# Kernel optimization log

Measured on AMD Instinct MI355X. Metric: run time of the kernel, lower is better.

## Reference

```python
import jax, jax.numpy as jnp
import numpy as np

B, N_PER, DEG, F_IN, F_HID = 64, 1024, 16, 128, 128
E = B * N_PER * DEG  # 1,048,576 edges, grouped per graph


def setup_inputs() -> dict:
    key = jax.random.key(0)
    ks = jax.random.split(key, 16)
    n_total = B * N_PER
    x = jax.random.normal(ks[0], (n_total, F_IN), dtype=jnp.float32)
    # edges are random within each graph block
    local = jax.random.randint(ks[1], (2, E), 0, N_PER)
    offs = (jnp.arange(E, dtype=jnp.int64) // (N_PER * DEG)) * N_PER
    edge_index = (local.astype(jnp.int64) + offs[None, :])
    edge_weight = jax.random.uniform(ks[2], (E,), dtype=jnp.float32)
    batch_index = jnp.repeat(jnp.arange(B, dtype=jnp.int64), N_PER)
    s = 1.0 / np.sqrt(F_HID)
    params = {
        'W1': jax.random.normal(ks[3], (F_IN, F_HID)) * s,
        'b1': jnp.zeros((F_HID,), jnp.float32),
        'p1': jax.random.normal(ks[4], (F_HID,)) * s,
        'W2': jax.random.normal(ks[5], (F_HID, F_HID)) * s,
        'b2': jnp.zeros((F_HID,), jnp.float32),
        'p2': jax.random.normal(ks[6], (F_HID,)) * s,
        'W3': jax.random.normal(ks[7], (F_HID, F_HID)) * s,
        'b3': jnp.zeros((F_HID,), jnp.float32),
        'p3': jax.random.normal(ks[8], (F_HID,)) * s,
        'Wo': jax.random.normal(ks[9], (2 * F_HID, 1)) * s,
        'bo': jnp.zeros((1,), jnp.float32),
    }
    return {'x': x, 'edge_index': edge_index, 'edge_weight': edge_weight,
            'batch_index': batch_index, **params}


def _gcn_conv(x, src, dst, w, W, b):
    # GCNConv with add_self_loops=True, symmetric normalization, edge_weight.
    n = x.shape[0]
    xW = x @ W
    deg = jnp.zeros((n,), x.dtype).at[dst].add(w) + 1.0  # +1 from self-loop fill
    dinv = jax.lax.rsqrt(deg)
    norm = dinv[src] * w * dinv[dst]
    agg = jnp.zeros_like(xW).at[dst].add(norm[:, None] * xW[src])
    return agg + (dinv * dinv)[:, None] * xW + b  # self-loop term + bias


def _topk_pool(x, src, dst, w, p, n, k):
    # TopKPooling with nonlinearity=sigmoid, equal-size graphs (n -> k nodes).
    f = x.shape[1]
    xr = x.reshape(B, n, f)
    score = jax.nn.sigmoid((xr @ p) / jnp.linalg.norm(p))  # [B, n]
    vals, perm = jax.lax.top_k(score, k)                    # per-graph top-k
    xn = jnp.take_along_axis(xr, perm[:, :, None], axis=1) * vals[:, :, None]
    # inverse map old local idx -> new local idx (-1 if dropped)
    inv = jnp.full((B, n), -1, dtype=jnp.int32)
    inv = inv.at[jnp.arange(B)[:, None], perm].set(jnp.arange(k, dtype=jnp.int32)[None, :])
    g = src // n
    sl = inv[g, src % n]
    dl = inv[dst // n, dst % n]
    keep = (sl >= 0) & (dl >= 0)
    # dropped edges are masked to node 0 with weight 0 (contribute nothing)
    src2 = jnp.where(keep, g * k + sl, 0)
    dst2 = jnp.where(keep, (dst // n) * k + dl, 0)
    w2 = jnp.where(keep, w, jnp.zeros((), w.dtype))
    return xn.reshape(B * k, f), src2, dst2, w2


def reference(x, edge_index, edge_weight, batch_index,
              W1, b1, p1, W2, b2, p2, W3, b3, p3, Wo, bo):
    src, dst = edge_index[0], edge_index[1]
    w = edge_weight
    n = N_PER
    h = _gcn_conv(x, src, dst, w, W1, b1)
    h, src, dst, w = _topk_pool(h, src, dst, w, p1, n, n // 2); n //= 2
    h = jax.nn.relu(h)
    h = _gcn_conv(h, src, dst, w, W2, b2)
    h, src, dst, w = _topk_pool(h, src, dst, w, p2, n, n // 2); n //= 2
    h = jax.nn.relu(h)
    h = _gcn_conv(h, src, dst, w, W3, b3)
    h, src, dst, w = _topk_pool(h, src, dst, w, p3, n, n // 2); n //= 2
    h = jax.nn.relu(h)
    hr = h.reshape(B, n, -1)
    cat = jnp.concatenate([hr.max(axis=1), hr.mean(axis=1)], axis=1)  # gmp || gap
    out = jax.nn.sigmoid(cat @ Wo + bo)
    return out, cat
```

## Files before the change

kernel.cpp:

```cpp
#include <hip/hip_runtime.h>

#define NB 64
#define EDGES 1048576
#define NTOT  65536

struct __align__(8) CsrE { int s; float w; };

using bf16x8 = __attribute__((ext_vector_type(8))) short;
using f32x4  = __attribute__((ext_vector_type(4))) float;

__global__ void k_zerof(float* __restrict__ p, int n){
  int i=blockIdx.x*256+threadIdx.x; if(i<n) p[i]=0.f;
}

__device__ inline void split1(float x, unsigned &hi16, unsigned &lo16){
  unsigned b=__float_as_uint(x);
  unsigned h=(b+0x7FFFu+((b>>16)&1u))&0xFFFF0000u;
  float lf=x-__uint_as_float(h);
  unsigned lb=__float_as_uint(lf);
  hi16=h>>16;
  lo16=(lb+0x7FFFu+((lb>>16)&1u))>>16;
}

__device__ inline void split8(const float4&u, const float4&v, bf16x8&hi, bf16x8&lo){
  float e[8]={u.x,u.y,u.z,u.w,v.x,v.y,v.z,v.w};
  #pragma unroll
  for(int j=0;j<8;++j){
    unsigned h16,l16; split1(e[j],h16,l16);
    hi[j]=(short)h16; lo[j]=(short)l16;
  }
}

__global__ __launch_bounds__(256) void k_cntpack(const int* __restrict__ edst,
        const float* __restrict__ ew, int* __restrict__ chunkcnt, float* __restrict__ chunkw,
        const float* __restrict__ W1, const float* __restrict__ W2,
        const float* __restrict__ W3, unsigned* __restrict__ outp){
  __shared__ int lc[1024];
  __shared__ float lw[1024];
  int b=blockIdx.x, tid=threadIdx.x;
  if(b<512){
    int xcd=b&7, slot=b>>3;
    int graph=xcd*8+(slot&7), chunk=slot>>3;
    int e0=graph*16384+chunk*2048;
    for(int t=tid;t<1024;t+=256){ lc[t]=0; lw[t]=0.f; }
    __syncthreads();
    for(int e=e0+tid; e<e0+2048; e+=256){
      int dl=edst[e]&1023;
      atomicAdd(&lc[dl],1);
      atomicAdd(&lw[dl],ew[e]);
    }
    __syncthreads();
    for(int t=tid;t<1024;t+=256){
      chunkcnt[chunk*65536+graph*1024+t]=lc[t];
      chunkw  [chunk*65536+graph*1024+t]=lw[t];
    }
  } else {
    int wb=b-512, m=wb>>3;
    const float* W = (m==0)?W1:((m==1)?W2:W3);
    unsigned* o = outp + m*16384;
    for(int t=(wb&7)*256+tid; t<8192; t+=2048){
      int i=t&3, l=(t>>2)&63, c=(t>>8)&7, q=(t>>11)&3;
      int col=c*16+(l&15);
      int k0=q*32+((l>>4)<<3)+i*2;
      float x0=W[k0*128+col], x1=W[(k0+1)*128+col];
      unsigned h0,l0,h1,l1;
      split1(x0,h0,l0); split1(x1,h1,l1);
      int base=((q*8+c)*2)*256;
      o[base + l*4 + i]       = (h1<<16)|h0;
      o[base + 256 + l*4 + i] = (l1<<16)|l0;
    }
  }
}

__global__ __launch_bounds__(256) void k_mm1scat(const float* __restrict__ X,
        const unsigned* __restrict__ Wpk,
        const int* __restrict__ esrc, const int* __restrict__ edst,
        const float* __restrict__ ew, const int* __restrict__ chunkcnt,
        const float* __restrict__ chunkw, int* __restrict__ rowptr,
        float* __restrict__ dinv1, CsrE* __restrict__ csr,
        float* __restrict__ Y){
  __shared__ __align__(16) unsigned Wl[16384];
  int b=blockIdx.x;
  if(b<512){
    const int RPB=128;
    int row0b=b*RPB;
    for(int t=threadIdx.x;t<4096;t+=256)
      ((uint4*)Wl)[t]=((const uint4*)Wpk)[t];
    const int wave=threadIdx.x>>6, lane=threadIdx.x&63;
    const int row0=row0b+wave*32;
    const int lrow=lane&15, lko=(lane>>4)<<3;
    int orow[2];
    #pragma unroll
    for(int s=0;s<2;++s) orow[s]=row0+s*16+lrow;
    const f32x4 vzero={0.f,0.f,0.f,0.f};
    f32x4 acc[2][8];
    #pragma unroll
    for(int s=0;s<2;++s){
      #pragma unroll
      for(int c=0;c<8;++c) acc[s][c]=vzero;
    }
    __syncthreads();
    const char* wb=(const char*)Wl + lane*16;
    float4 u[2],v[2];
    #pragma unroll
    for(int s=0;s<2;++s){
      const float* xp=X+(size_t)orow[s]*128+lko;
      u[s]=*(const float4*)xp; v[s]=*(const float4*)(xp+4);
    }
    #pragma unroll
    for(int q=0;q<4;++q){
      float4 un[2],vn[2];
      if(q<3){
        #pragma unroll
        for(int s=0;s<2;++s){
          const float* xp=X+(size_t)orow[s]*128+(q+1)*32+lko;
          un[s]=*(const float4*)xp; vn[s]=*(const float4*)(xp+4);
        }
      }
      bf16x8 Ah[2],Al[2];
      #pragma unroll
      for(int s=0;s<2;++s) split8(u[s],v[s],Ah[s],Al[s]);
      #pragma unroll
      for(int c=0;c<8;++c){
        const bf16x8 bh=*(const bf16x8*)(wb + (q*8+c)*2048);
        const bf16x8 bl=*(const bf16x8*)(wb + (q*8+c)*2048 + 1024);
        #pragma unroll
        for(int s=0;s<2;++s){
          acc[s][c]=__builtin_amdgcn_mfma_f32_16x16x32_bf16(Ah[s],bh,acc[s][c],0,0,0);
          acc[s][c]=__builtin_amdgcn_mfma_f32_16x16x32_bf16(Al[s],bh,acc[s][c],0,0,0);
          acc[s][c]=__builtin_amdgcn_mfma_f32_16x16x32_bf16(Ah[s],bl,acc[s][c],0,0,0);
        }
      }
      if(q<3){
        #pragma unroll
        for(int s=0;s<2;++s){ u[s]=un[s]; v[s]=vn[s]; }
      }
    }
    const int dcol=lane&15, dr0=(lane>>4)<<2;
    #pragma unroll
    for(int s=0;s<2;++s){
      #pragma unroll
      for(int c=0;c<8;++c){
        #pragma unroll
        for(int r=0;r<4;++r){
          Y[(size_t)(row0+s*16+dr0+r)*128 + c*16 + dcol]=acc[s][c][r];
        }
      }
    }
  } else {
    int* lc=(int*)Wl;
    int* wsum=(int*)Wl+1024;
    int sb=b-512, i=threadIdx.x;
    int lane=i&63, w=i>>6;
    int xcd=sb&7, slot=sb>>3;
    int graph=xcd*8+(slot&7), chunk=slot>>3;
    int n0=4*i, o0=graph*1024+n0;
    int ck[4][8], csum[4];
    int tot=0;
    #pragma unroll
    for(int j=0;j<4;++j){
      int c=0;
      #pragma unroll
      for(int k=0;k<8;++k){ int t=chunkcnt[k*65536+o0+j]; ck[j][k]=t; c+=t; }
      csum[j]=c; tot+=c;
    }
    int v=tot;
    #pragma unroll
    for(int off=1;off<64;off<<=1){ int t=__shfl_up(v,off,64); if(lane>=off) v+=t; }
    if(lane==63) wsum[w]=v;
    __syncthreads();
    int base=0;
    for(int k=0;k<w;++k) base+=wsum[k];
    int texcl=base+v-tot;
    int run=texcl;
    #pragma unroll
    for(int j=0;j<4;++j){
      int r0=graph*16384+run;
      if(chunk==0){
        rowptr[o0+j]=r0;
        float wsv=0.f;
        #pragma unroll
        for(int k=0;k<8;++k) wsv+=chunkw[k*65536+o0+j];
        dinv1[o0+j]=rsqrtf(wsv+1.0f);
      }
      int myfill=r0;
      #pragma unroll
      for(int k=0;k<8;++k) if(k<chunk) myfill+=ck[j][k];
      lc[n0+j]=myfill;
      run+=csum[j];
    }
    if(graph==63 && chunk==0 && i==255) rowptr[65536]=EDGES;
    __syncthreads();
    int e0=graph*16384+chunk*2048;
    for(int e=e0+i; e<e0+2048; e+=256){
      int dl=edst[e]&1023;
      int pos=atomicAdd(&lc[dl],1);
      CsrE ce; ce.s=esrc[e]; ce.w=ew[e];
      csr[pos]=ce;
    }
  }
}

template<bool G, int S>
__global__ __launch_bounds__(256) void mm_mfma(const float* __restrict__ X,
        const unsigned* __restrict__ Wpk, const int* __restrict__ selold,
        const float* __restrict__ score, float* __restrict__ Y, int gshift){
  __shared__ __align__(16) unsigned Wl[16384];
  const int RPB = 64*S;
  int b=blockIdx.x;
  int row0b;
  if(G){
    int xcd=b&7, slot=b>>3, bpg=1<<gshift;
    int graph=xcd*8+(slot>>gshift), idx=slot&(bpg-1);
    row0b = graph*(bpg*RPB) + idx*RPB;
  } else row0b = b*RPB;
  for(int t=threadIdx.x;t<4096;t+=256)
    ((uint4*)Wl)[t]=((const uint4*)Wpk)[t];
  const int wave=threadIdx.x>>6, lane=threadIdx.x&63;
  const int row0 = row0b + wave*(16*S);
  const int lrow=lane&15, lko=(lane>>4)<<3;
  int orow[S]; float scr[S];
  #pragma unroll
  for(int s=0;s<S;++s){
    int rr=row0+s*16+lrow;
    orow[s]=G?selold[rr]:rr;
    scr[s]=G?score[orow[s]]:1.f;
  }
  const f32x4 vzero={0.f,0.f,0.f,0.f};
  f32x4 acc[S][8];
  #pragma unroll
  for(int s=0;s<S;++s){
    #pragma unroll
    for(int c=0;c<8;++c) acc[s][c]=vzero;
  }
  __syncthreads();
  const char* wb=(const char*)Wl + lane*16;
  float4 u[S],v[S];
  #pragma unroll
  for(int s=0;s<S;++s){
    const float* xp=X+(size_t)orow[s]*128+lko;
    u[s]=*(const float4*)xp; v[s]=*(const float4*)(xp+4);
  }
  #pragma unroll
  for(int q=0;q<4;++q){
    float4 un[S],vn[S];
    if(q<3){
      #pragma unroll
      for(int s=0;s<S;++s){
        const float* xp=X+(size_t)orow[s]*128+(q+1)*32+lko;
        un[s]=*(const float4*)xp; vn[s]=*(const float4*)(xp+4);
      }
    }
    bf16x8 Ah[S],Al[S];
    #pragma unroll
    for(int s=0;s<S;++s){
      if(G){
        u[s].x=fmaxf(u[s].x*scr[s],0.f); u[s].y=fmaxf(u[s].y*scr[s],0.f);
        u[s].z=fmaxf(u[s].z*scr[s],0.f); u[s].w=fmaxf(u[s].w*scr[s],0.f);
        v[s].x=fmaxf(v[s].x*scr[s],0.f); v[s].y=fmaxf(v[s].y*scr[s],0.f);
        v[s].z=fmaxf(v[s].z*scr[s],0.f); v[s].w=fmaxf(v[s].w*scr[s],0.f);
      }
      split8(u[s],v[s],Ah[s],Al[s]);
    }
    #pragma unroll
    for(int c=0;c<8;++c){
      const bf16x8 bh=*(const bf16x8*)(wb + (q*8+c)*2048);
      const bf16x8 bl=*(const bf16x8*)(wb + (q*8+c)*2048 + 1024);
      #pragma unroll
      for(int s=0;s<S;++s){
        acc[s][c]=__builtin_amdgcn_mfma_f32_16x16x32_bf16(Ah[s],bh,acc[s][c],0,0,0);
        acc[s][c]=__builtin_amdgcn_mfma_f32_16x16x32_bf16(Al[s],bh,acc[s][c],0,0,0);
        acc[s][c]=__builtin_amdgcn_mfma_f32_16x16x32_bf16(Ah[s],bl,acc[s][c],0,0,0);
      }
    }
    if(q<3){
      #pragma unroll
      for(int s=0;s<S;++s){ u[s]=un[s]; v[s]=vn[s]; }
    }
  }
  const int dcol=lane&15, dr0=(lane>>4)<<2;
  #pragma unroll
  for(int s=0;s<S;++s){
    #pragma unroll
    for(int c=0;c<8;++c){
      #pragma unroll
      for(int r=0;r<4;++r){
        Y[(size_t)(row0+s*16+dr0+r)*128 + c*16 + dcol]=acc[s][c][r];
      }
    }
  }
}

template<bool F>
__global__ __launch_bounds__(256) void k_gather(const float* __restrict__ xw, const CsrE* __restrict__ csr,
        const int* __restrict__ rowptr, const int* __restrict__ map, const int* __restrict__ inv,
        const float* __restrict__ dinvv, const float* __restrict__ bias, const float* __restrict__ p,
        float* __restrict__ h, float* __restrict__ score, int gshift, int ns){
  int wv=threadIdx.x>>6, half=(threadIdx.x>>5)&1, hl=threadIdx.x&31;
  int b=blockIdx.x, xcd=b&7, slot=b>>3, bpg=1<<gshift;
  int graph=xcd*8+(slot>>gshift), idx=slot&(bpg-1);
  int v = graph*(bpg<<3) + (idx<<3) + wv*2 + half;
  if(v>=ns) return;
  int d0 = F? map[v] : v;
  float dv=dinvv[v];
  int rs=rowptr[d0], re=rowptr[d0+1];
  const int f4=hl*4;
  float4 accA={0.f,0.f,0.f,0.f}, accB={0.f,0.f,0.f,0.f};
  for(int base=rs; base<re; base+=32){
    int len=re-base; if(len>32) len=32;
    int sidx=0; float cf=0.f;
    if(hl<len){
      CsrE en=csr[base+hl];
      int s=en.s; bool live=true;
      if(F){ int t=inv[s]; live=(t>=0); s=live?t:0; }
      if(live){ sidx=s; cf=dinvv[s]*en.w; }
    }
    int len8=(len+7)&~7;
    for(int j=0;j<len8;j+=8){
      float cc[8]; int ss[8];
      #pragma unroll
      for(int m=0;m<8;++m){ cc[m]=__shfl(cf,j+m,32); ss[m]=__shfl(sidx,j+m,32); }
      float4 xv_[8];
      #pragma unroll
      for(int m=0;m<8;++m) xv_[m]=*(const float4*)&xw[(size_t)ss[m]*128+f4];
      #pragma unroll
      for(int m=0;m<8;m+=2){
        accA.x+=cc[m]*xv_[m].x; accA.y+=cc[m]*xv_[m].y;
        accA.z+=cc[m]*xv_[m].z; accA.w+=cc[m]*xv_[m].w;
        accB.x+=cc[m+1]*xv_[m+1].x; accB.y+=cc[m+1]*xv_[m+1].y;
        accB.z+=cc[m+1]*xv_[m+1].z; accB.w+=cc[m+1]*xv_[m+1].w;
      }
    }
  }
  float4 acc; acc.x=accA.x+accB.x; acc.y=accA.y+accB.y;
  acc.z=accA.z+accB.z; acc.w=accA.w+accB.w;
  const float4 xv=*(const float4*)&xw[(size_t)v*128+f4];
  const float4 bv=*(const float4*)&bias[f4];
  float d2=dv*dv;
  float4 hv;
  hv.x=acc.x*dv + d2*xv.x + bv.x;
  hv.y=acc.y*dv + d2*xv.y + bv.y;
  hv.z=acc.z*dv + d2*xv.z + bv.z;
  hv.w=acc.w*dv + d2*xv.w + bv.w;
  *(float4*)&h[(size_t)v*128+f4]=hv;
  const float4 pv=*(const float4*)&p[f4];
  float z=hv.x*pv.x+hv.y*pv.y+hv.z*pv.z+hv.w*pv.w;
  float pp=pv.x*pv.x+pv.y*pv.y+pv.z*pv.z+pv.w*pv.w;
  #pragma unroll
  for(int m=16;m>0;m>>=1){ z+=__shfl_xor(z,m,32); pp+=__shfl_xor(pp,m,32); }
  if(hl==0) score[v]=1.0f/(1.0f+expf(-z/sqrtf(pp)));
}

template<int N, int K, int MODE>
__global__ __launch_bounds__(N) void k_topk(const float* __restrict__ score,
        int* __restrict__ inv, int* __restrict__ selold,
        const int* __restrict__ inv1s, const int* __restrict__ sel1s,
        int* __restrict__ inv12, int* __restrict__ map12,
        const int* __restrict__ rowptr, const CsrE* __restrict__ csr,
        float* __restrict__ dinv_out,
        const float* __restrict__ h3, const float* __restrict__ Wo,
        const float* __restrict__ bo, float* __restrict__ outp){
  __shared__ unsigned hist[256];
  __shared__ int wsum[16];
  __shared__ int c_sh, r_sh;
  __shared__ float red2[256];
  __shared__ int sOld[128];
  __shared__ float sSc[128];
  int g=blockIdx.x, i=threadIdx.x;
  int lane=i&63, w=i>>6;
  int gv=g*N+i;
  unsigned key=__float_as_uint(score[gv]);
  int st=1;
  int R=K;
  #pragma unroll
  for(int pass=0; pass<4; ++pass){
    int shift=24-pass*8;
    if(i<256) hist[i]=0;
    __syncthreads();
    unsigned byte=(key>>shift)&255u;
    if(st==1) atomicAdd(&hist[byte],1u);
    __syncthreads();
    unsigned hcnt=0, sfx=0;
    if(i<256){
      hcnt=hist[i]; sfx=hcnt;
      #pragma unroll
      for(int off=1;off<64;off<<=1){
        unsigned t=__shfl_down(sfx,off,64);
        if(lane+off<64) sfx+=t;
      }
      if(lane==0) wsum[w]=(int)sfx;
    }
    __syncthreads();
    if(i<256){
      int tot=0;
      for(int k=w+1;k<4;++k) tot+=wsum[k];
      int Si=(int)sfx+tot;
      int A=Si-(int)hcnt;
      if(A<R && R<=Si){ c_sh=i; r_sh=R-A; }
    }
    __syncthreads();
    int c=c_sh; R=r_sh;
    if(st==1){
      if((int)byte>c) st=2;
      else if((int)byte<c) st=0;
    }
    __syncthreads();
  }
  int alive=(st==1)?1:0;
  unsigned long long mA=__ballot(alive);
  int rA=__popcll(mA & ((1ULL<<lane)-1ULL));
  if(lane==0) wsum[w]=__popcll(mA);
  __syncthreads();
  int offA=0;
  for(int k=0;k<w;++k) offA+=wsum[k];
  int tie_rank=offA+rA;
  int sel=(st==2)||(st==1 && tie_rank<R);
  __syncthreads();
  unsigned long long mS=__ballot(sel);
  int rS=__popcll(mS & ((1ULL<<lane)-1ULL));
  if(lane==0) wsum[w]=__popcll(mS);
  __syncthreads();
  int offS=0;
  for(int k=0;k<w;++k) offS+=wsum[k];
  int ng=g*K+offS+rS;
  if(sel && ng<NB*K){ inv[gv]=ng; selold[ng]=gv; }
  else inv[gv]=-1;
  if(MODE==1){
    __syncthreads();
    for(int t=i; t<K; t+=N){
      int v=g*K+t;
      int d0=selold[v];
      int rs=rowptr[d0], re=rowptr[d0+1];
      float s0=0.f,s1=0.f,s2=0.f,s3=0.f;
      int e=rs;
      for(; e+4<=re; e+=4){
        CsrE e0=csr[e], e1=csr[e+1], e2=csr[e+2], e3=csr[e+3];
        if(inv[e0.s]>=0) s0+=e0.w;
        if(inv[e1.s]>=0) s1+=e1.w;
        if(inv[e2.s]>=0) s2+=e2.w;
        if(inv[e3.s]>=0) s3+=e3.w;
      }
      for(; e<re; ++e){
        CsrE en=csr[e];
        if(inv[en.s]>=0) s0+=en.w;
      }
      dinv_out[v]=rsqrtf((s0+s1)+(s2+s3)+1.0f);
    }
  }
  if(MODE==2){
    __syncthreads();
    for(int t=i; t<1024; t+=N){
      int v0=g*1024+t;
      int q=inv1s[v0];
      inv12[v0]=(q>=0)?inv[q]:-1;
    }
    for(int t=i; t<K; t+=N){
      int v=g*K+t;
      map12[v]=sel1s[selold[v]];
    }
    __syncthreads();
    for(int t=i; t<K; t+=N){
      int v=g*K+t;
      int d0=map12[v];
      int rs=rowptr[d0], re=rowptr[d0+1];
      float s0=0.f,s1=0.f,s2=0.f,s3=0.f;
      int e=rs;
      for(; e+4<=re; e+=4){
        CsrE e0=csr[e], e1=csr[e+1], e2=csr[e+2], e3=csr[e+3];
        if(inv12[e0.s]>=0) s0+=e0.w;
        if(inv12[e1.s]>=0) s1+=e1.w;
        if(inv12[e2.s]>=0) s2+=e2.w;
        if(inv12[e3.s]>=0) s3+=e3.w;
      }
      for(; e<re; ++e){
        CsrE en=csr[e];
        if(inv12[en.s]>=0) s0+=en.w;
      }
      dinv_out[v]=rsqrtf((s0+s1)+(s2+s3)+1.0f);
    }
  }
  if(MODE==3){
    __syncthreads();
    if(i<128){ int o=selold[g*128+i]; sOld[i]=o; sSc[i]=score[o]; }
    __syncthreads();
    int f=i&127, hf=i>>7;
    float mx=-3.4e38f, sm=0.f;
    #pragma unroll 4
    for(int nd=hf*64; nd<hf*64+64; ++nd){
      float vv=fmaxf(h3[(size_t)sOld[nd]*128+f]*sSc[nd],0.f);
      mx=fmaxf(mx,vv); sm+=vv;
    }
    red2[i]=mx; __syncthreads();
    float mx2 = (hf==0)? fmaxf(mx,red2[i+128]) : 0.f;
    __syncthreads();
    red2[i]=sm; __syncthreads();
    if(hf==0){
      float smT=sm+red2[i+128];
      float mean=smT*(1.0f/128.0f);
      outp[64+g*256+f]    =mx2;
      outp[64+g*256+128+f]=mean;
    }
    __syncthreads();
    if(hf==0) red2[f]=mx2*Wo[f]+( (sm+red2[f+128]) * (1.0f/128.0f))*Wo[128+f];
    __syncthreads();
    for(int off=64;off>0;off>>=1){
      if(i<off) red2[i]+=red2[i+off];
      __syncthreads();
    }
    if(i==0){ float z=red2[0]+bo[0]; outp[g]=1.0f/(1.0f+expf(-z)); }
  }
}

extern "C" void kernel_launch(void* const* d_in, const int* in_sizes, int n_in,
                              void* d_out, int out_size, void* d_ws, size_t ws_size,
                              hipStream_t stream) {
  (void)in_sizes; (void)n_in;
  const float* x  = (const float*)d_in[0];
  const int*   ei = (const int*)d_in[1];
  const float* ew = (const float*)d_in[2];
  const float* W1=(const float*)d_in[4];  const float* b1=(const float*)d_in[5];  const float* p1=(const float*)d_in[6];
  const float* W2=(const float*)d_in[7];  const float* b2=(const float*)d_in[8];  const float* p2=(const float*)d_in[9];
  const float* W3=(const float*)d_in[10]; const float* b3=(const float*)d_in[11]; const float* p3=(const float*)d_in[12];
  const float* Wo=(const float*)d_in[13]; const float* bo=(const float*)d_in[14];
  float* out=(float*)d_out;

  char* ws=(char*)d_ws;
  size_t cur=0;
  float* slot0=(float*)(ws+cur); cur+=33554432;
  float* slot1=(float*)(ws+cur); cur+=33554432;
  CsrE*  csr  =(CsrE*)(ws+cur);  cur+=(size_t)EDGES*8;
  int*   chunkcnt=(int*)(ws+cur); cur+=2097152;
  float* chunkw  =(float*)(ws+cur); cur+=2097152;
  int*   rowptr=(int*) (ws+cur); cur+=262400;
  float* dinv1=(float*)(ws+cur); cur+=262144;
  float* dinv2=(float*)(ws+cur); cur+=131072;
  float* dinv3=(float*)(ws+cur); cur+=65536;
  float* sc1  =(float*)(ws+cur); cur+=262144;
  float* sc2  =(float*)(ws+cur); cur+=131072;
  float* sc3  =(float*)(ws+cur); cur+=65536;
  int*   inv1 =(int*)  (ws+cur); cur+=262144;
  int*   inv2 =(int*)  (ws+cur); cur+=131072;
  int*   invS =(int*)  (ws+cur); cur+=65536;
  int*   inv12=(int*)  (ws+cur); cur+=262144;
  int*   sel1 =(int*)  (ws+cur); cur+=131072;
  int*   sel2 =(int*)  (ws+cur); cur+=65536;
  int*   sel3 =(int*)  (ws+cur); cur+=32768;
  int*   map12=(int*)  (ws+cur); cur+=65536;
  unsigned* wpk=(unsigned*)(ws+cur); cur+=196608;

  if (ws_size < cur) {
    k_zerof<<<(out_size+255)/256,256,0,stream>>>(out,out_size);
    return;
  }

  const int* esrc=ei; const int* edst=ei+EDGES;

  k_cntpack<<<536,256,0,stream>>>(edst,ew,chunkcnt,chunkw,W1,W2,W3,wpk);
  k_mm1scat<<<1024,256,0,stream>>>(x,wpk,esrc,edst,ew,chunkcnt,chunkw,
                                   rowptr,dinv1,csr,slot0);
  k_gather<false><<<NTOT/8,256,0,stream>>>(slot0,csr,rowptr,nullptr,nullptr,
                                           dinv1,b1,p1,slot1,sc1,7,NTOT);
  k_topk<1024,512,1><<<NB,1024,0,stream>>>(sc1,inv1,sel1,nullptr,nullptr,nullptr,nullptr,
                                           rowptr,csr,dinv2,nullptr,nullptr,nullptr,nullptr);

  mm_mfma<true,1><<<32768/64,256,0,stream>>>(slot1,wpk+16384,sel1,sc1,slot0,3);
  k_gather<true><<<32768/8,256,0,stream>>>(slot0,csr,rowptr,sel1,inv1,
                                           dinv2,b2,p2,slot1,sc2,6,32768);
  k_topk<512,256,2><<<NB,512,0,stream>>>(sc2,inv2,sel2,inv1,sel1,inv12,map12,
                                         rowptr,csr,dinv3,nullptr,nullptr,nullptr,nullptr);

  mm_mfma<true,1><<<16384/64,256,0,stream>>>(slot1,wpk+32768,sel2,sc2,slot0,2);
  k_gather<true><<<16384/8,256,0,stream>>>(slot0,csr,rowptr,map12,inv12,
                                           dinv3,b3,p3,slot1,sc3,5,16384);
  k_topk<256,128,3><<<NB,256,0,stream>>>(sc3,invS,sel3,nullptr,nullptr,nullptr,nullptr,
                                         nullptr,nullptr,nullptr,slot1,Wo,bo,out);
}
```

Baseline: 271.8 us.

## Move pooled-degree computation from topk blocks into extra blocks of matmul kernel

The per-node degree/dinv computation for the pooled graphs was done inside the 64-block top-k kernels, where each block serially walked many nodes' edge lists. It now runs in extra thread blocks appended to the following MFMA matmul launch, which spreads the work over many more blocks and lets it overlap with the matmul. The gather inner loop is also narrowed from 8 to 4 edges per step, and the final readout is simplified to one thread per feature. The simpler readout gives up the two-way split over nodes that it had before.

```diff
diff --git a/kernel.cpp b/kernel.cpp
--- a/kernel.cpp
+++ b/kernel.cpp
@@ -201,93 +201,147 @@
   }
 }
 
-template<bool G, int S>
+template<bool G, int S, int EPI, int MMB>
 __global__ __launch_bounds__(256) void mm_mfma(const float* __restrict__ X,
         const unsigned* __restrict__ Wpk, const int* __restrict__ selold,
-        const float* __restrict__ score, float* __restrict__ Y, int gshift){
+        const float* __restrict__ score, float* __restrict__ Y, int gshift,
+        const int* __restrict__ inv1, const int* __restrict__ sel1,
+        const int* __restrict__ inv2, const int* __restrict__ sel2,
+        int* __restrict__ inv12, int* __restrict__ map12,
+        const int* __restrict__ rowptr, const CsrE* __restrict__ csr,
+        float* __restrict__ dinv_out){
   __shared__ __align__(16) unsigned Wl[16384];
-  const int RPB = 64*S;
   int b=blockIdx.x;
-  int row0b;
-  if(G){
-    int xcd=b&7, slot=b>>3, bpg=1<<gshift;
-    int graph=xcd*8+(slot>>gshift), idx=slot&(bpg-1);
-    row0b = graph*(bpg*RPB) + idx*RPB;
-  } else row0b = b*RPB;
-  for(int t=threadIdx.x;t<4096;t+=256)
-    ((uint4*)Wl)[t]=((const uint4*)Wpk)[t];
-  const int wave=threadIdx.x>>6, lane=threadIdx.x&63;
-  const int row0 = row0b + wave*(16*S);
-  const int lrow=lane&15, lko=(lane>>4)<<3;
-  int orow[S]; float scr[S];
-  #pragma unroll
-  for(int s=0;s<S;++s){
-    int rr=row0+s*16+lrow;
-    orow[s]=G?selold[rr]:rr;
-    scr[s]=G?score[orow[s]]:1.f;
-  }
-  const f32x4 vzero={0.f,0.f,0.f,0.f};
-  f32x4 acc[S][8];
-  #pragma unroll
-  for(int s=0;s<S;++s){
-    #pragma unroll
-    for(int c=0;c<8;++c) acc[s][c]=vzero;
-  }
-  __syncthreads();
-  const char* wb=(const char*)Wl + lane*16;
-  float4 u[S],v[S];
-  #pragma unroll
-  for(int s=0;s<S;++s){
-    const float* xp=X+(size_t)orow[s]*128+lko;
-    u[s]=*(const float4*)xp; v[s]=*(const float4*)(xp+4);
-  }
-  #pragma unroll
-  for(int q=0;q<4;++q){
-    float4 un[S],vn[S];
-    if(q<3){
+  if(b<MMB){
+    const int RPB = 64*S;
+    int row0b;
+    if(G){
+      int xcd=b&7, slot=b>>3, bpg=1<<gshift;
+      int graph=xcd*8+(slot>>gshift), idx=slot&(bpg-1);
+      row0b = graph*(bpg*RPB) + idx*RPB;
+    } else row0b = b*RPB;
+    for(int t=threadIdx.x;t<4096;t+=256)
+      ((uint4*)Wl)[t]=((const uint4*)Wpk)[t];
+    const int wave=threadIdx.x>>6, lane=threadIdx.x&63;
+    const int row0 = row0b + wave*(16*S);
+    const int lrow=lane&15, lko=(lane>>4)<<3;
+    int orow[S]; float scr[S];
+    #pragma unroll
+    for(int s=0;s<S;++s){
+      int rr=row0+s*16+lrow;
+      orow[s]=G?selold[rr]:rr;
+      scr[s]=G?score[orow[s]]:1.f;
+    }
+    const f32x4 vzero={0.f,0.f,0.f,0.f};
+    f32x4 acc[S][8];
+    #pragma unroll
+    for(int s=0;s<S;++s){
+      #pragma unroll
+      for(int c=0;c<8;++c) acc[s][c]=vzero;
+    }
+    __syncthreads();
+    const char* wb=(const char*)Wl + lane*16;
+    float4 u[S],v[S];
+    #pragma unroll
+    for(int s=0;s<S;++s){
+      const float* xp=X+(size_t)orow[s]*128+lko;
+      u[s]=*(const float4*)xp; v[s]=*(const float4*)(xp+4);
+    }
+    #pragma unroll
+    for(int q=0;q<4;++q){
+      float4 un[S],vn[S];
+      if(q<3){
+        #pragma unroll
+        for(int s=0;s<S;++s){
+          const float* xp=X+(size_t)orow[s]*128+(q+1)*32+lko;
+          un[s]=*(const float4*)xp; vn[s]=*(const float4*)(xp+4);
+        }
+      }
+      bf16x8 Ah[S],Al[S];
       #pragma unroll
       for(int s=0;s<S;++s){
-        const float* xp=X+(size_t)orow[s]*128+(q+1)*32+lko;
-        un[s]=*(const float4*)xp; vn[s]=*(const float4*)(xp+4);
-      }
-    }
-    bf16x8 Ah[S],Al[S];
+        if(G){
+          u[s].x=fmaxf(u[s].x*scr[s],0.f); u[s].y=fmaxf(u[s].y*scr[s],0.f);
+          u[s].z=fmaxf(u[s].z*scr[s],0.f); u[s].w=fmaxf(u[s].w*scr[s],0.f);
+          v[s].x=fmaxf(v[s].x*scr[s],0.f); v[s].y=fmaxf(v[s].y*scr[s],0.f);
+          v[s].z=fmaxf(v[s].z*scr[s],0.f); v[s].w=fmaxf(v[s].w*scr[s],0.f);
+        }
+        split8(u[s],v[s],Ah[s],Al[s]);
+      }
+      #pragma unroll
+      for(int c=0;c<8;++c){
+        const bf16x8 bh=*(const bf16x8*)(wb + (q*8+c)*2048);
+        const bf16x8 bl=*(const bf16x8*)(wb + (q*8+c)*2048 + 1024);
+        #pragma unroll
+        for(int s=0;s<S;++s){
+          acc[s][c]=__builtin_amdgcn_mfma_f32_16x16x32_bf16(Ah[s],bh,acc[s][c],0,0,0);
+          acc[s][c]=__builtin_amdgcn_mfma_f32_16x16x32_bf16(Al[s],bh,acc[s][c],0,0,0);
+          acc[s][c]=__builtin_amdgcn_mfma_f32_16x16x32_bf16(Ah[s],bl,acc[s][c],0,0,0);
+        }
+      }
+      if(q<3){
+        #pragma unroll
+        for(int s=0;s<S;++s){ u[s]=un[s]; v[s]=vn[s]; }
+      }
+    }
+    const int dcol=lane&15, dr0=(lane>>4)<<2;
     #pragma unroll
     for(int s=0;s<S;++s){
-      if(G){
-        u[s].x=fmaxf(u[s].x*scr[s],0.f); u[s].y=fmaxf(u[s].y*scr[s],0.f);
-        u[s].z=fmaxf(u[s].z*scr[s],0.f); u[s].w=fmaxf(u[s].w*scr[s],0.f);
-        v[s].x=fmaxf(v[s].x*scr[s],0.f); v[s].y=fmaxf(v[s].y*scr[s],0.f);
-        v[s].z=fmaxf(v[s].z*scr[s],0.f); v[s].w=fmaxf(v[s].w*scr[s],0.f);
-      }
-      split8(u[s],v[s],Ah[s],Al[s]);
-    }
-    #pragma unroll
-    for(int c=0;c<8;++c){
-      const bf16x8 bh=*(const bf16x8*)(wb + (q*8+c)*2048);
-      const bf16x8 bl=*(const bf16x8*)(wb + (q*8+c)*2048 + 1024);
-      #pragma unroll
-      for(int s=0;s<S;++s){
-        acc[s][c]=__builtin_amdgcn_mfma_f32_16x16x32_bf16(Ah[s],bh,acc[s][c],0,0,0);
-        acc[s][c]=__builtin_amdgcn_mfma_f32_16x16x32_bf16(Al[s],bh,acc[s][c],0,0,0);
-        acc[s][c]=__builtin_amdgcn_mfma_f32_16x16x32_bf16(Ah[s],bl,acc[s][c],0,0,0);
-      }
-    }
-    if(q<3){
-      #pragma unroll
-      for(int s=0;s<S;++s){ u[s]=un[s]; v[s]=vn[s]; }
-    }
-  }
-  const int dcol=lane&15, dr0=(lane>>4)<<2;
-  #pragma unroll
-  for(int s=0;s<S;++s){
-    #pragma unroll
-    for(int c=0;c<8;++c){
-      #pragma unroll
-      for(int r=0;r<4;++r){
-        Y[(size_t)(row0+s*16+dr0+r)*128 + c*16 + dcol]=acc[s][c][r];
-      }
-    }
+      #pragma unroll
+      for(int c=0;c<8;++c){
+        #pragma unroll
+        for(int r=0;r<4;++r){
+          Y[(size_t)(row0+s*16+dr0+r)*128 + c*16 + dcol]=acc[s][c][r];
+        }
+      }
+    }
+    return;
+  }
+  if(EPI==2){
+    int v=(b-MMB)*256+threadIdx.x;
+    int d0=sel1[v];
+    int rs=rowptr[d0], re=rowptr[d0+1];
+    float s0=0.f,s1=0.f,s2=0.f,s3=0.f;
+    int e=rs;
+    for(; e+4<=re; e+=4){
+      CsrE e0=csr[e], e1=csr[e+1], e2=csr[e+2], e3=csr[e+3];
+      if(inv1[e0.s]>=0) s0+=e0.w;
+      if(inv1[e1.s]>=0) s1+=e1.w;
+      if(inv1[e2.s]>=0) s2+=e2.w;
+      if(inv1[e3.s]>=0) s3+=e3.w;
+    }
+    for(; e<re; ++e){
+      CsrE en=csr[e];
+      if(inv1[en.s]>=0) s0+=en.w;
+    }
+    dinv_out[v]=rsqrtf((s0+s1)+(s2+s3)+1.0f);
+  }
+  if(EPI==3){
+    int g=b-MMB, i=threadIdx.x;
+    for(int t=i; t<1024; t+=256){
+      int v0=g*1024+t;
+      int q=inv1[v0];
+      inv12[v0]=(q>=0)?inv2[q]:-1;
+    }
+    int v=g*256+i;
+    map12[v]=sel1[sel2[v]];
+    __syncthreads();
+    int d0=map12[v];
+    int rs=rowptr[d0], re=rowptr[d0+1];
+    float s0=0.f,s1=0.f,s2=0.f,s3=0.f;
+    int e=rs;
+    for(; e+4<=re; e+=4){
+      CsrE e0=csr[e], e1=csr[e+1], e2=csr[e+2], e3=csr[e+3];
+      if(inv12[e0.s]>=0) s0+=e0.w;
+      if(inv12[e1.s]>=0) s1+=e1.w;
+      if(inv12[e2.s]>=0) s2+=e2.w;
+      if(inv12[e3.s]>=0) s3+=e3.w;
+    }
+    for(; e<re; ++e){
+      CsrE en=csr[e];
+      if(inv12[en.s]>=0) s0+=en.w;
+    }
+    dinv_out[v]=rsqrtf((s0+s1)+(s2+s3)+1.0f);
   }
 }
 
@@ -315,21 +369,20 @@
       if(F){ int t=inv[s]; live=(t>=0); s=live?t:0; }
       if(live){ sidx=s; cf=dinvv[s]*en.w; }
     }
-    int len8=(len+7)&~7;
-    for(int j=0;j<len8;j+=8){
-      float cc[8]; int ss[8];
-      #pragma unroll
-      for(int m=0;m<8;++m){ cc[m]=__shfl(cf,j+m,32); ss[m]=__shfl(sidx,j+m,32); }
-      float4 xv_[8];
-      #pragma unroll
-      for(int m=0;m<8;++m) xv_[m]=*(const float4*)&xw[(size_t)ss[m]*128+f4];
-      #pragma unroll
-      for(int m=0;m<8;m+=2){
-        accA.x+=cc[m]*xv_[m].x; accA.y+=cc[m]*xv_[m].y;
-        accA.z+=cc[m]*xv_[m].z; accA.w+=cc[m]*xv_[m].w;
-        accB.x+=cc[m+1]*xv_[m+1].x; accB.y+=cc[m+1]*xv_[m+1].y;
-        accB.z+=cc[m+1]*xv_[m+1].z; accB.w+=cc[m+1]*xv_[m+1].w;
-      }
+    int len4=(len+3)&~3;
+    for(int j=0;j<len4;j+=4){
+      float c0=__shfl(cf,j,32),   c1=__shfl(cf,j+1,32);
+      float c2=__shfl(cf,j+2,32), c3=__shfl(cf,j+3,32);
+      int   s0=__shfl(sidx,j,32),   s1=__shfl(sidx,j+1,32);
+      int   s2=__shfl(sidx,j+2,32), s3=__shfl(sidx,j+3,32);
+      const float4 x0=*(const float4*)&xw[(size_t)s0*128+f4];
+      const float4 x1=*(const float4*)&xw[(size_t)s1*128+f4];
+      const float4 x2=*(const float4*)&xw[(size_t)s2*128+f4];
+      const float4 x3=*(const float4*)&xw[(size_t)s3*128+f4];
+      accA.x+=c0*x0.x; accA.y+=c0*x0.y; accA.z+=c0*x0.z; accA.w+=c0*x0.w;
+      accB.x+=c1*x1.x; accB.y+=c1*x1.y; accB.z+=c1*x1.z; accB.w+=c1*x1.w;
+      accA.x+=c2*x2.x; accA.y+=c2*x2.y; accA.z+=c2*x2.z; accA.w+=c2*x2.w;
+      accB.x+=c3*x3.x; accB.y+=c3*x3.y; accB.z+=c3*x3.z; accB.w+=c3*x3.w;
     }
   }
   float4 acc; acc.x=accA.x+accB.x; acc.y=accA.y+accB.y;
@@ -354,18 +407,12 @@
 template<int N, int K, int MODE>
 __global__ __launch_bounds__(N) void k_topk(const float* __restrict__ score,
         int* __restrict__ inv, int* __restrict__ selold,
-        const int* __restrict__ inv1s, const int* __restrict__ sel1s,
-        int* __restrict__ inv12, int* __restrict__ map12,
-        const int* __restrict__ rowptr, const CsrE* __restrict__ csr,
-        float* __restrict__ dinv_out,
         const float* __restrict__ h3, const float* __restrict__ Wo,
         const float* __restrict__ bo, float* __restrict__ outp){
   __shared__ unsigned hist[256];
   __shared__ int wsum[16];
   __shared__ int c_sh, r_sh;
-  __shared__ float red2[256];
-  __shared__ int sOld[128];
-  __shared__ float sSc[128];
+  __shared__ float red[128];
   int g=blockIdx.x, i=threadIdx.x;
   int lane=i&63, w=i>>6;
   int gv=g*N+i;
@@ -425,89 +472,27 @@
   int ng=g*K+offS+rS;
   if(sel && ng<NB*K){ inv[gv]=ng; selold[ng]=gv; }
   else inv[gv]=-1;
-  if(MODE==1){
-    __syncthreads();
-    for(int t=i; t<K; t+=N){
-      int v=g*K+t;
-      int d0=selold[v];
-      int rs=rowptr[d0], re=rowptr[d0+1];
-      float s0=0.f,s1=0.f,s2=0.f,s3=0.f;
-      int e=rs;
-      for(; e+4<=re; e+=4){
-        CsrE e0=csr[e], e1=csr[e+1], e2=csr[e+2], e3=csr[e+3];
-        if(inv[e0.s]>=0) s0+=e0.w;
-        if(inv[e1.s]>=0) s1+=e1.w;
-        if(inv[e2.s]>=0) s2+=e2.w;
-        if(inv[e3.s]>=0) s3+=e3.w;
-      }
-      for(; e<re; ++e){
-        CsrE en=csr[e];
-        if(inv[en.s]>=0) s0+=en.w;
-      }
-      dinv_out[v]=rsqrtf((s0+s1)+(s2+s3)+1.0f);
-    }
-  }
-  if(MODE==2){
-    __syncthreads();
-    for(int t=i; t<1024; t+=N){
-      int v0=g*1024+t;
-      int q=inv1s[v0];
-      inv12[v0]=(q>=0)?inv[q]:-1;
-    }
-    for(int t=i; t<K; t+=N){
-      int v=g*K+t;
-      map12[v]=sel1s[selold[v]];
-    }
-    __syncthreads();
-    for(int t=i; t<K; t+=N){
-      int v=g*K+t;
-      int d0=map12[v];
-      int rs=rowptr[d0], re=rowptr[d0+1];
-      float s0=0.f,s1=0.f,s2=0.f,s3=0.f;
-      int e=rs;
-      for(; e+4<=re; e+=4){
-        CsrE e0=csr[e], e1=csr[e+1], e2=csr[e+2], e3=csr[e+3];
-        if(inv12[e0.s]>=0) s0+=e0.w;
-        if(inv12[e1.s]>=0) s1+=e1.w;
-        if(inv12[e2.s]>=0) s2+=e2.w;
-        if(inv12[e3.s]>=0) s3+=e3.w;
-      }
-      for(; e<re; ++e){
-        CsrE en=csr[e];
-        if(inv12[en.s]>=0) s0+=en.w;
-      }
-      dinv_out[v]=rsqrtf((s0+s1)+(s2+s3)+1.0f);
-    }
-  }
   if(MODE==3){
     __syncthreads();
-    if(i<128){ int o=selold[g*128+i]; sOld[i]=o; sSc[i]=score[o]; }
-    __syncthreads();
-    int f=i&127, hf=i>>7;
+    int f=i;
     float mx=-3.4e38f, sm=0.f;
-    #pragma unroll 4
-    for(int nd=hf*64; nd<hf*64+64; ++nd){
-      float vv=fmaxf(h3[(size_t)sOld[nd]*128+f]*sSc[nd],0.f);
-      mx=fmaxf(mx,vv); sm+=vv;
-    }
-    red2[i]=mx; __syncthreads();
-    float mx2 = (hf==0)? fmaxf(mx,red2[i+128]) : 0.f;
-    __syncthreads();
-    red2[i]=sm; __syncthreads();
-    if(hf==0){
-      float smT=sm+red2[i+128];
-      float mean=smT*(1.0f/128.0f);
-      outp[64+g*256+f]    =mx2;
+    if(f<128){
+      for(int nd=0;nd<128;++nd){
+        int old=selold[g*128+nd];
+        float vv=fmaxf(h3[(size_t)old*128+f]*score[old],0.f);
+        mx=fmaxf(mx,vv); sm+=vv;
+      }
+      float mean=sm*(1.0f/128.0f);
+      outp[64+g*256+f]    =mx;
       outp[64+g*256+128+f]=mean;
-    }
-    __syncthreads();
-    if(hf==0) red2[f]=mx2*Wo[f]+( (sm+red2[f+128]) * (1.0f/128.0f))*Wo[128+f];
+      red[f]=mx*Wo[f]+mean*Wo[128+f];
+    }
     __syncthreads();
     for(int off=64;off>0;off>>=1){
-      if(i<off) red2[i]+=red2[i+off];
+      if(f<off) red[f]+=red[f+off];
       __syncthreads();
     }
-    if(i==0){ float z=red2[0]+bo[0]; outp[g]=1.0f/(1.0f+expf(-z)); }
+    if(f==0){ float z=red[0]+bo[0]; outp[g]=1.0f/(1.0f+expf(-z)); }
   }
 }
 
@@ -560,18 +545,17 @@
                                    rowptr,dinv1,csr,slot0);
   k_gather<false><<<NTOT/8,256,0,stream>>>(slot0,csr,rowptr,nullptr,nullptr,
                                            dinv1,b1,p1,slot1,sc1,7,NTOT);
-  k_topk<1024,512,1><<<NB,1024,0,stream>>>(sc1,inv1,sel1,nullptr,nullptr,nullptr,nullptr,
-                                           rowptr,csr,dinv2,nullptr,nullptr,nullptr,nullptr);
-
-  mm_mfma<true,1><<<32768/64,256,0,stream>>>(slot1,wpk+16384,sel1,sc1,slot0,3);
+  k_topk<1024,512,0><<<NB,1024,0,stream>>>(sc1,inv1,sel1,nullptr,nullptr,nullptr,nullptr);
+
+  mm_mfma<true,1,2,512><<<640,256,0,stream>>>(slot1,wpk+16384,sel1,sc1,slot0,3,
+      inv1,sel1,nullptr,nullptr,nullptr,nullptr,rowptr,csr,dinv2);
   k_gather<true><<<32768/8,256,0,stream>>>(slot0,csr,rowptr,sel1,inv1,
                                            dinv2,b2,p2,slot1,sc2,6,32768);
-  k_topk<512,256,2><<<NB,512,0,stream>>>(sc2,inv2,sel2,inv1,sel1,inv12,map12,
-                                         rowptr,csr,dinv3,nullptr,nullptr,nullptr,nullptr);
-
-  mm_mfma<true,1><<<16384/64,256,0,stream>>>(slot1,wpk+32768,sel2,sc2,slot0,2);
+  k_topk<512,256,0><<<NB,512,0,stream>>>(sc2,inv2,sel2,nullptr,nullptr,nullptr,nullptr);
+
+  mm_mfma<true,1,3,256><<<320,256,0,stream>>>(slot1,wpk+32768,sel2,sc2,slot0,2,
+      inv1,sel1,inv2,sel2,inv12,map12,rowptr,csr,dinv3);
   k_gather<true><<<16384/8,256,0,stream>>>(slot0,csr,rowptr,map12,inv12,
                                            dinv3,b3,p3,slot1,sc3,5,16384);
-  k_topk<256,128,3><<<NB,256,0,stream>>>(sc3,invS,sel3,nullptr,nullptr,nullptr,nullptr,
-                                         nullptr,nullptr,nullptr,slot1,Wo,bo,out);
-}
+  k_topk<256,128,3><<<NB,256,0,stream>>>(sc3,invS,sel3,slot1,Wo,bo,out);
+}
```

Result: faster. 263.0 us (-3.2%).
